# Kernel optimization log

Measured on AMD Instinct MI355X. Metric: run time of the kernel, lower is better.

## Reference

```python
import jax, jax.numpy as jnp
import numpy as np

L, N, D_IN = 4, 2048, 1024
H, DH = 8, 64
INNER = H * DH          # 512
D_OUT = D_IN            # out_dim defaults to input_dim
SCALE = DH ** -0.5


def setup_inputs() -> dict:
    key = jax.random.key(0)
    ks = jax.random.split(key, 7)
    x = jax.random.normal(ks[0], (L, N, D_IN), jnp.float32)
    # torch Linear weights are [out_features, in_features]; xavier-ish scale
    Wq = jax.random.normal(ks[1], (INNER, D_IN), jnp.float32) * 0.03
    Wk = jax.random.normal(ks[2], (INNER, D_IN), jnp.float32) * 0.03
    Wv = jax.random.normal(ks[3], (INNER, D_IN), jnp.float32) * 0.03
    Wo = jax.random.normal(ks[4], (D_OUT, INNER), jnp.float32) * 0.03
    bo = jnp.zeros((D_OUT,), jnp.float32)
    # boolean key-padding mask [L, n]; ensure at least one valid key per row
    mask = jax.random.uniform(ks[5], (L, N)) < 0.9
    mask = mask.at[:, 0].set(True)
    return {"x": x, "Wq": Wq, "Wk": Wk, "Wv": Wv, "Wo": Wo, "bo": bo, "mask": mask}


def reference(x, Wq, Wk, Wv, Wo, bo, mask):
    # projections (Linear: y = x @ W^T), split heads: L n (h d) -> l h n d
    def split_heads(t):
        return t.reshape(L, N, H, DH).transpose(0, 2, 1, 3)

    q = split_heads(jnp.einsum('lnd,ed->lne', x, Wq))
    k = split_heads(jnp.einsum('lnd,ed->lne', x, Wk))  # context defaults to x
    v = split_heads(jnp.einsum('lnd,ed->lne', x, Wv))

    sim = jnp.einsum('lhnd,lhmd->lhnm', q, k) * SCALE   # [L,H,N,N]
    neg = -jnp.finfo(sim.dtype).max
    sim = jnp.where(mask[:, None, None, :], sim, neg)   # mask over key dim
    attn = jax.nn.softmax(sim, axis=-1)

    out = jnp.einsum('lhnm,lhmd->lhnd', attn, v)        # [L,H,N,DH]
    out = out.transpose(0, 2, 1, 3).reshape(L, N, INNER)
    return out @ Wo.T + bo                               # [L,N,D_OUT]
```

## Files before the change

kernel.cpp:

```cpp
#include <hip/hip_runtime.h>
#include <hip/hip_bf16.h>

#define L_DIM 4
#define N_DIM 2048
#define DIN   1024
#define H_DIM 8
#define DH    64
#define INNER 512

typedef __attribute__((ext_vector_type(8))) short short8;
typedef __attribute__((ext_vector_type(4))) float f32x4;

__device__ __forceinline__ unsigned short f2bf(float f) {
  unsigned u = __builtin_bit_cast(unsigned, f);
  u += 0x7fffu + ((u >> 16) & 1u);
  return (unsigned short)(u >> 16);
}

__device__ __forceinline__ unsigned cvtpk(float a, float b) {
  unsigned r;
  asm("v_cvt_pk_bf16_f32 %0, %1, %2" : "=v"(r) : "v"(a), "v"(b));
  return r;
}

__device__ __forceinline__ float fexp2(float x) {
  float r;
  asm("v_exp_f32 %0, %1" : "=v"(r) : "v"(x));
  return r;
}

typedef __attribute__((address_space(3))) unsigned int lds_uint;
typedef const __attribute__((address_space(1))) unsigned int glob_uint;
__device__ __forceinline__ void gl_lds16(const unsigned short* g,
                                         unsigned short* l) {
  __builtin_amdgcn_global_load_lds((glob_uint*)g, (lds_uint*)l, 16, 0, 0);
}

__global__ void cast_all(const float* __restrict__ x,
                         const float* __restrict__ wq,
                         const float* __restrict__ wk,
                         const float* __restrict__ wv,
                         const float* __restrict__ wo,
                         unsigned short* __restrict__ xb,
                         unsigned short* __restrict__ w3,
                         unsigned short* __restrict__ wob,
                         const unsigned char* __restrict__ mraw,
                         float* __restrict__ bias) {
  __shared__ int votes[2];
  int bid = blockIdx.x, t = threadIdx.x;
  if (bid == 10240) {
    if (t < 2) votes[t] = 0;
    __syncthreads();
    const unsigned int* m32 = (const unsigned int*)mraw;
    int anyf = 0, any8 = 0;
    for (int i = t; i < 2048; i += 256) {
      unsigned w = m32[i];
      if (w == 0x3f800000u) anyf = 1;
      if (w & 0xffffff00u) any8 = 1;
    }
    if (anyf) atomicOr(&votes[0], 1);
    if (any8) atomicOr(&votes[1], 1);
    __syncthreads();
    int fmt = votes[0] ? 2 : (votes[1] ? 1 : 0);
    for (int i = t; i < L_DIM * N_DIM; i += 256) {
      int mv;
      if (fmt == 2)      mv = ((const float*)mraw)[i] != 0.0f;
      else if (fmt == 1) mv = mraw[i] != 0;
      else               mv = ((const int*)mraw)[i] != 0;
      bias[i] = mv ? 0.0f : -1e30f;
    }
    return;
  }
  int i = (bid * 256 + t) * 4;
  const float* src; unsigned short* dst; int off;
  if (i < 8388608)      { src = x;  dst = xb;           off = i; }
  else if (i < 8912896) { src = wq; dst = w3;           off = i - 8388608; }
  else if (i < 9437184) { src = wk; dst = w3 + 524288;  off = i - 8912896; }
  else if (i < 9961472) { src = wv; dst = w3 + 1048576; off = i - 9437184; }
  else                  { src = wo; dst = wob;          off = i - 9961472; }
  float4 f = *(const float4*)(src + off);
  ushort4 o4;
  o4.x = f2bf(f.x); o4.y = f2bf(f.y); o4.z = f2bf(f.z); o4.w = f2bf(f.w);
  *(ushort4*)(dst + off) = o4;
}

__launch_bounds__(256, 3)
__global__ void gemm_qkv(const unsigned short* __restrict__ xb,
                         const unsigned short* __restrict__ w3,
                         unsigned short* __restrict__ qp,
                         unsigned short* __restrict__ kp,
                         unsigned short* __restrict__ vtp) {
  __shared__ __align__(16) unsigned short Sh[16384];
  const int tid = threadIdx.x, lane = tid & 63, wid = tid >> 6;
  const int l16 = lane & 15, quad = lane >> 4;
  const int wm = wid >> 1, wn = wid & 1;
  const int m0 = blockIdx.x * 128, n0 = blockIdx.y * 128;

  int aoff[2], boff[2], lofs[2];
#pragma unroll
  for (int it = 0; it < 2; ++it) {
    int c = it * 256 + wid * 64 + lane;
    int row = c >> 2, kseg = c & 3;
    aoff[it] = (m0 + row) * DIN + kseg * 8;
    boff[it] = (n0 + row) * DIN + kseg * 8;
    lofs[it] = (it * 256 + wid * 64) * 8;
  }

#pragma unroll
  for (int it = 0; it < 2; ++it) {
    gl_lds16(&xb[aoff[it]], &Sh[lofs[it]]);
    gl_lds16(&w3[boff[it]], &Sh[8192 + lofs[it]]);
  }

  f32x4 acc[4][4] = {};
  for (int t = 0; t < 32; ++t) {
    const int buf = t & 1;
    __syncthreads();
    if (t < 31) {
      int kt2 = (t + 1) * 32, b2 = buf ^ 1;
#pragma unroll
      for (int it = 0; it < 2; ++it) {
        gl_lds16(&xb[aoff[it] + kt2], &Sh[b2 * 4096 + lofs[it]]);
        gl_lds16(&w3[boff[it] + kt2], &Sh[8192 + b2 * 4096 + lofs[it]]);
      }
    }
    const unsigned short* As = &Sh[buf * 4096];
    const unsigned short* Bs = &Sh[8192 + buf * 4096];
    short8 af[4], bf[4];
#pragma unroll
    for (int mt = 0; mt < 4; ++mt)
      af[mt] = *(const short8*)&As[(wm * 64 + mt * 16 + l16) * 32 + quad * 8];
#pragma unroll
    for (int nt = 0; nt < 4; ++nt)
      bf[nt] = *(const short8*)&Bs[(wn * 64 + nt * 16 + l16) * 32 + quad * 8];
#pragma unroll
    for (int mt = 0; mt < 4; ++mt)
#pragma unroll
      for (int nt = 0; nt < 4; ++nt)
        acc[mt][nt] = __builtin_amdgcn_mfma_f32_16x16x32_bf16(
            af[mt], bf[nt], acc[mt][nt], 0, 0, 0);
  }
  if (blockIdx.y >= 8) {
    const int l = m0 >> 11, mloc = m0 & 2047;
#pragma unroll
    for (int chunk = 0; chunk < 2; ++chunk) {
      __syncthreads();
      if (wn == chunk) {
#pragma unroll
        for (int mt = 0; mt < 4; ++mt)
#pragma unroll
          for (int nt = 0; nt < 4; ++nt) {
            int col = nt * 16 + l16;
            int rowb = wm * 64 + mt * 16 + quad * 4;
            ushort4 pv;
            pv.x = f2bf(acc[mt][nt][0]);
            pv.y = f2bf(acc[mt][nt][1]);
            pv.z = f2bf(acc[mt][nt][2]);
            pv.w = f2bf(acc[mt][nt][3]);
            *(ushort4*)&Sh[col * 136 + rowb] = pv;
          }
      }
      __syncthreads();
      int hh = ((n0 + chunk * 64) & 511) >> 6;
#pragma unroll
      for (int it = 0; it < 4; ++it) {
        int c = it * 256 + tid;
        int cl = c >> 4, seg = c & 15;
        short8 vv = *(const short8*)&Sh[cl * 136 + seg * 8];
        *(short8*)&vtp[((size_t)((l * H_DIM + hh) * DH + cl)) * N_DIM + mloc +
                       seg * 8] = vv;
      }
    }
  } else {
    const int l = m0 >> 11, nloc = m0 & 2047;
    const int hbase = (n0 & 511) >> 6;
    unsigned short* dstp = (n0 >> 9) ? kp : qp;
#pragma unroll
    for (int chunk = 0; chunk < 2; ++chunk) {
      __syncthreads();
      if (wn == chunk) {
#pragma unroll
        for (int mt = 0; mt < 4; ++mt)
#pragma unroll
          for (int nt = 0; nt < 4; ++nt) {
            int col = nt * 16 + l16;
            int rowb = wm * 64 + mt * 16 + quad * 4;
#pragma unroll
            for (int r = 0; r < 4; ++r)
              Sh[(rowb + r) * 72 + col] = f2bf(acc[mt][nt][r]);
          }
      }
      __syncthreads();
      int hh = hbase + chunk;
      unsigned short* db =
          dstp + ((size_t)(l * H_DIM + hh) * N_DIM + nloc) * DH;
#pragma unroll
      for (int it = 0; it < 4; ++it) {
        int c = it * 256 + tid;
        int row = c >> 3, seg = c & 7;
        short8 vv = *(const short8*)&Sh[row * 72 + seg * 8];
        *(short8*)&db[row * DH + seg * 8] = vv;
      }
    }
  }
}

#define PW_S 64
__launch_bounds__(128, 2)
__global__ void attn_kernel(const unsigned short* __restrict__ qg,
                            const unsigned short* __restrict__ kg,
                            const unsigned short* __restrict__ vtg,
                            const float* __restrict__ bias,
                            unsigned short* __restrict__ aout) {
  __shared__ __align__(16) unsigned short Ks[2][64 * 64];
  __shared__ __align__(16) unsigned short Vs[2][64 * 64];
  __shared__ __align__(16) unsigned short Pw[64 * PW_S];
  const int tid = threadIdx.x, lane = tid & 63, wid = tid >> 6;
  const int l16 = lane & 15, quad = lane >> 4;
  const int bid = blockIdx.x;
  const int xcd = bid & 7, j = bid >> 3;
  const int lh = xcd * 4 + (j >> 5);
  const int q0 = (j & 31) << 6;
  const int l = lh >> 3, h = lh & 7;
  const unsigned short* Qb = qg + (size_t)lh * N_DIM * DH;
  const unsigned short* Kb = kg + (size_t)lh * N_DIM * DH;
  const unsigned short* Vt = vtg + (size_t)lh * DH * N_DIM;
  const float* bl = bias + l * N_DIM;

  short8 qf[2][2];
#pragma unroll
  for (int mt = 0; mt < 2; ++mt)
#pragma unroll
    for (int ks = 0; ks < 2; ++ks)
      qf[mt][ks] = *(const short8*)&Qb[(q0 + wid * 32 + mt * 16 + l16) * DH +
                                       ks * 32 + quad * 8];

  f32x4 o[2][4] = {};
  float lsum[2] = {0.f, 0.f};

  int kof[4], ldsb[4];
  size_t vof[4];
#pragma unroll
  for (int it = 0; it < 4; ++it) {
    int cb = it * 128 + wid * 64, c = cb + lane;
    int rr = c >> 3, sl = c & 7, gs = (sl + rr) & 7;
    kof[it] = rr * DH + gs * 8;
    vof[it] = (size_t)rr * N_DIM + gs * 8;
    ldsb[it] = cb * 8;
  }

#pragma unroll
  for (int it = 0; it < 4; ++it) {
    gl_lds16(&Kb[kof[it]], &Ks[0][ldsb[it]]);
    gl_lds16(&Vt[vof[it]], &Vs[0][ldsb[it]]);
  }

  for (int t = 0; t < 32; ++t) {
    const int kv = t << 6, buf = t & 1;
    __syncthreads();
    if (t < 31) {
      int kv2 = kv + 64, b2 = buf ^ 1;
#pragma unroll
      for (int it = 0; it < 4; ++it) {
        gl_lds16(&Kb[(kv2 << 6) + kof[it]], &Ks[b2][ldsb[it]]);
        gl_lds16(&Vt[vof[it] + kv2], &Vs[b2][ldsb[it]]);
      }
    }
    const unsigned short* Kst = Ks[buf];
    const unsigned short* Vst = Vs[buf];

    f32x4 sc[2][4] = {};
#pragma unroll
    for (int nt = 0; nt < 4; ++nt)
#pragma unroll
      for (int ks = 0; ks < 2; ++ks) {
        int s = (ks * 4 + quad - l16) & 7;
        short8 kf = *(const short8*)&Kst[(nt * 16 + l16) * 64 + s * 8];
#pragma unroll
        for (int mt = 0; mt < 2; ++mt)
          sc[mt][nt] = __builtin_amdgcn_mfma_f32_16x16x32_bf16(
              kf, qf[mt][ks], sc[mt][nt], 0, 0, 0);
      }
#pragma unroll
    for (int mt = 0; mt < 2; ++mt) {
      unsigned short* pr = &Pw[(wid * 32 + mt * 16 + l16) * PW_S];
#pragma unroll
      for (int nt = 0; nt < 4; ++nt) {
        float4 b4 = *(const float4*)&bl[kv + nt * 16 + quad * 4];
        float p0 = fexp2(fmaf(sc[mt][nt][0], 0.18033688011f, b4.x));
        float p1 = fexp2(fmaf(sc[mt][nt][1], 0.18033688011f, b4.y));
        float p2 = fexp2(fmaf(sc[mt][nt][2], 0.18033688011f, b4.z));
        float p3 = fexp2(fmaf(sc[mt][nt][3], 0.18033688011f, b4.w));
        lsum[mt] += (p0 + p1) + (p2 + p3);
        uint2 pk = make_uint2(cvtpk(p0, p1), cvtpk(p2, p3));
        int gk = nt * 2 + (quad >> 1);
        int s = (gk + l16) & 7;
        *(uint2*)&pr[s * 8 + (quad & 1) * 4] = pk;
      }
    }
#pragma unroll
    for (int g = 0; g < 2; ++g) {
      short8 pa[2];
#pragma unroll
      for (int mt = 0; mt < 2; ++mt) {
        int sp = (g * 4 + quad + l16) & 7;
        pa[mt] = *(const short8*)&Pw[(wid * 32 + mt * 16 + l16) * PW_S +
                                     sp * 8];
      }
#pragma unroll
      for (int nt = 0; nt < 4; ++nt) {
        int dd = nt * 16 + l16;
        int sv2 = (g * 4 + quad - l16) & 7;
        short8 vb = *(const short8*)&Vst[dd * 64 + sv2 * 8];
#pragma unroll
        for (int mt = 0; mt < 2; ++mt)
          o[mt][nt] = __builtin_amdgcn_mfma_f32_16x16x32_bf16(
              pa[mt], vb, o[mt][nt], 0, 0, 0);
      }
    }
  }
#pragma unroll
  for (int mt = 0; mt < 2; ++mt) {
    lsum[mt] += __shfl_xor(lsum[mt], 16);
    lsum[mt] += __shfl_xor(lsum[mt], 32);
  }
#pragma unroll
  for (int mt = 0; mt < 2; ++mt)
#pragma unroll
    for (int r = 0; r < 4; ++r) {
      float inv = 1.f / __shfl(lsum[mt], quad * 4 + r);
      int row = q0 + wid * 32 + mt * 16 + quad * 4 + r;
#pragma unroll
      for (int nt = 0; nt < 4; ++nt)
        aout[(size_t)(l * N_DIM + row) * INNER + h * DH + nt * 16 + l16] =
            f2bf(o[mt][nt][r] * inv);
    }
}

__launch_bounds__(256, 4)
__global__ void gemm_out(const unsigned short* __restrict__ a,
                         const unsigned short* __restrict__ wo,
                         const float* __restrict__ bo,
                         float* __restrict__ out) {
  __shared__ __align__(16) unsigned short Sh[12288];
  const int tid = threadIdx.x, lane = tid & 63, wid = tid >> 6;
  const int l16 = lane & 15, quad = lane >> 4;
  const int wm = wid >> 1, wn = wid & 1;
  const int m0 = blockIdx.x * 128, n0 = blockIdx.y * 64;

  int aoff[2], lofsA[2];
#pragma unroll
  for (int it = 0; it < 2; ++it) {
    int c = it * 256 + wid * 64 + lane;
    int row = c >> 2, kseg = c & 3;
    aoff[it] = (m0 + row) * INNER + kseg * 8;
    lofsA[it] = (it * 256 + wid * 64) * 8;
  }
  int boff, lofsB;
  {
    int c = wid * 64 + lane;
    int row = c >> 2, kseg = c & 3;
    boff = (n0 + row) * INNER + kseg * 8;
    lofsB = (wid * 64) * 8;
  }

#pragma unroll
  for (int it = 0; it < 2; ++it)
    gl_lds16(&a[aoff[it]], &Sh[lofsA[it]]);
  gl_lds16(&wo[boff], &Sh[8192 + lofsB]);

  f32x4 acc[4][2] = {};
  for (int t = 0; t < 16; ++t) {
    const int buf = t & 1;
    __syncthreads();
    if (t < 15) {
      int kt2 = (t + 1) * 32, b2 = buf ^ 1;
#pragma unroll
      for (int it = 0; it < 2; ++it)
        gl_lds16(&a[aoff[it] + kt2], &Sh[b2 * 4096 + lofsA[it]]);
      gl_lds16(&wo[boff + kt2], &Sh[8192 + b2 * 2048 + lofsB]);
    }
    const unsigned short* As = &Sh[buf * 4096];
    const unsigned short* Bs = &Sh[8192 + buf * 2048];
    short8 af[4], bf[2];
#pragma unroll
    for (int mt = 0; mt < 4; ++mt)
      af[mt] = *(const short8*)&As[(wm * 64 + mt * 16 + l16) * 32 + quad * 8];
#pragma unroll
    for (int nt = 0; nt < 2; ++nt)
      bf[nt] = *(const short8*)&Bs[(wn * 32 + nt * 16 + l16) * 32 + quad * 8];
#pragma unroll
    for (int mt = 0; mt < 4; ++mt)
#pragma unroll
      for (int nt = 0; nt < 2; ++nt)
        acc[mt][nt] = __builtin_amdgcn_mfma_f32_16x16x32_bf16(
            af[mt], bf[nt], acc[mt][nt], 0, 0, 0);
  }
#pragma unroll
  for (int mt = 0; mt < 4; ++mt)
#pragma unroll
    for (int nt = 0; nt < 2; ++nt)
#pragma unroll
      for (int r = 0; r < 4; ++r) {
        int grow = m0 + wm * 64 + mt * 16 + quad * 4 + r;
        int gcol = n0 + wn * 32 + nt * 16 + l16;
        out[(size_t)grow * DIN + gcol] = acc[mt][nt][r] + bo[gcol];
      }
}

extern "C" void kernel_launch(void* const* d_in, const int* in_sizes, int n_in,
                              void* d_out, int out_size, void* d_ws,
                              size_t ws_size, hipStream_t stream) {
  const float* x  = (const float*)d_in[0];
  const float* Wq = (const float*)d_in[1];
  const float* Wk = (const float*)d_in[2];
  const float* Wv = (const float*)d_in[3];
  const float* Wo = (const float*)d_in[4];
  const float* bo = (const float*)d_in[5];
  const unsigned char* mask = (const unsigned char*)d_in[6];
  float* out = (float*)d_out;

  char* ws = (char*)d_ws;
  unsigned short* xb  = (unsigned short*)(ws + 0);
  unsigned short* w3  = (unsigned short*)(ws + 16777216);
  unsigned short* wob = (unsigned short*)(ws + 19922944);
  unsigned short* q   = (unsigned short*)(ws + 20971520);
  unsigned short* k   = (unsigned short*)(ws + 29360128);
  unsigned short* vt  = (unsigned short*)(ws + 37748736);
  unsigned short* att = (unsigned short*)(ws + 46137344);
  float* bias         = (float*)(ws + 54525952);

  cast_all<<<10241, 256, 0, stream>>>(x, Wq, Wk, Wv, Wo, xb, w3, wob, mask,
                                      bias);
  gemm_qkv<<<dim3(64, 12), 256, 0, stream>>>(xb, w3, q, k, vt);
  attn_kernel<<<1024, 128, 0, stream>>>(q, k, vt, bias, att);
  gemm_out<<<dim3(64, 16), 256, 0, stream>>>(att, wob, bo, out);
}
```

Baseline: 218.0 us.

## Halve attention query and key/value tiles to double block count and occupancy

Shrinks the attention block from 64 queries to 32 (16 per wave) and the key/value tile from 64 to 32, doubling the grid to 2048 blocks. It raises occupancy to 4 blocks per CU and cuts LDS and register use per block. In exchange each K/V tile is reused by half as many queries, so global and LDS traffic for K/V doubles and the loop runs twice as many barrier iterations.

```diff
diff --git a/kernel.cpp b/kernel.cpp
--- a/kernel.cpp
+++ b/kernel.cpp
@@ -205,63 +205,64 @@
   }
 }
 
-#define PW_S 64
-__launch_bounds__(128, 2)
+#define KVB 32
+#define PW_S 32
+__launch_bounds__(128, 4)
 __global__ void attn_kernel(const unsigned short* __restrict__ qg,
                             const unsigned short* __restrict__ kg,
                             const unsigned short* __restrict__ vtg,
                             const float* __restrict__ bias,
                             unsigned short* __restrict__ aout) {
-  __shared__ __align__(16) unsigned short Ks[2][64 * 64];
-  __shared__ __align__(16) unsigned short Vs[2][64 * 64];
-  __shared__ __align__(16) unsigned short Pw[64 * PW_S];
+  __shared__ __align__(16) unsigned short Ks[2][KVB * 64];
+  __shared__ __align__(16) unsigned short Vs[2][64 * KVB];
+  __shared__ __align__(16) unsigned short Pw[32 * PW_S];
   const int tid = threadIdx.x, lane = tid & 63, wid = tid >> 6;
   const int l16 = lane & 15, quad = lane >> 4;
   const int bid = blockIdx.x;
   const int xcd = bid & 7, j = bid >> 3;
-  const int lh = xcd * 4 + (j >> 5);
-  const int q0 = (j & 31) << 6;
+  const int lh = xcd * 4 + (j >> 6);
+  const int q0 = (j & 63) << 5;
   const int l = lh >> 3, h = lh & 7;
   const unsigned short* Qb = qg + (size_t)lh * N_DIM * DH;
   const unsigned short* Kb = kg + (size_t)lh * N_DIM * DH;
   const unsigned short* Vt = vtg + (size_t)lh * DH * N_DIM;
   const float* bl = bias + l * N_DIM;
 
-  short8 qf[2][2];
-#pragma unroll
-  for (int mt = 0; mt < 2; ++mt)
-#pragma unroll
-    for (int ks = 0; ks < 2; ++ks)
-      qf[mt][ks] = *(const short8*)&Qb[(q0 + wid * 32 + mt * 16 + l16) * DH +
-                                       ks * 32 + quad * 8];
-
-  f32x4 o[2][4] = {};
-  float lsum[2] = {0.f, 0.f};
-
-  int kof[4], ldsb[4];
-  size_t vof[4];
-#pragma unroll
-  for (int it = 0; it < 4; ++it) {
-    int cb = it * 128 + wid * 64, c = cb + lane;
-    int rr = c >> 3, sl = c & 7, gs = (sl + rr) & 7;
-    kof[it] = rr * DH + gs * 8;
-    vof[it] = (size_t)rr * N_DIM + gs * 8;
-    ldsb[it] = cb * 8;
-  }
-
-#pragma unroll
-  for (int it = 0; it < 4; ++it) {
+  short8 qf[2];
+#pragma unroll
+  for (int ks = 0; ks < 2; ++ks)
+    qf[ks] = *(const short8*)&Qb[(q0 + wid * 16 + l16) * DH + ks * 32 +
+                                 quad * 8];
+
+  f32x4 o[4] = {};
+  float lsum = 0.f;
+
+  int kof[2], vof0[2], ldsb[2];
+  size_t vof[2];
+#pragma unroll
+  for (int it = 0; it < 2; ++it) {
+    int c = it * 128 + wid * 64 + lane;
+    int key = c >> 3, sl = c & 7, gs = (sl + key) & 7;
+    kof[it] = key * DH + gs * 8;
+    int d = c >> 2, sv = c & 3, gv = (sv + d) & 3;
+    vof[it] = (size_t)d * N_DIM + gv * 8;
+    ldsb[it] = c * 8;
+  }
+  (void)vof0;
+
+#pragma unroll
+  for (int it = 0; it < 2; ++it) {
     gl_lds16(&Kb[kof[it]], &Ks[0][ldsb[it]]);
     gl_lds16(&Vt[vof[it]], &Vs[0][ldsb[it]]);
   }
 
-  for (int t = 0; t < 32; ++t) {
-    const int kv = t << 6, buf = t & 1;
+  for (int t = 0; t < 64; ++t) {
+    const int kv = t << 5, buf = t & 1;
     __syncthreads();
-    if (t < 31) {
-      int kv2 = kv + 64, b2 = buf ^ 1;
-#pragma unroll
-      for (int it = 0; it < 4; ++it) {
+    if (t < 63) {
+      int kv2 = kv + KVB, b2 = buf ^ 1;
+#pragma unroll
+      for (int it = 0; it < 2; ++it) {
         gl_lds16(&Kb[(kv2 << 6) + kof[it]], &Ks[b2][ldsb[it]]);
         gl_lds16(&Vt[vof[it] + kv2], &Vs[b2][ldsb[it]]);
       }
@@ -269,72 +270,54 @@
     const unsigned short* Kst = Ks[buf];
     const unsigned short* Vst = Vs[buf];
 
-    f32x4 sc[2][4] = {};
-#pragma unroll
-    for (int nt = 0; nt < 4; ++nt)
+    f32x4 sc[2] = {};
+#pragma unroll
+    for (int nt = 0; nt < 2; ++nt)
 #pragma unroll
       for (int ks = 0; ks < 2; ++ks) {
         int s = (ks * 4 + quad - l16) & 7;
         short8 kf = *(const short8*)&Kst[(nt * 16 + l16) * 64 + s * 8];
-#pragma unroll
-        for (int mt = 0; mt < 2; ++mt)
-          sc[mt][nt] = __builtin_amdgcn_mfma_f32_16x16x32_bf16(
-              kf, qf[mt][ks], sc[mt][nt], 0, 0, 0);
-      }
-#pragma unroll
-    for (int mt = 0; mt < 2; ++mt) {
-      unsigned short* pr = &Pw[(wid * 32 + mt * 16 + l16) * PW_S];
-#pragma unroll
-      for (int nt = 0; nt < 4; ++nt) {
-        float4 b4 = *(const float4*)&bl[kv + nt * 16 + quad * 4];
-        float p0 = fexp2(fmaf(sc[mt][nt][0], 0.18033688011f, b4.x));
-        float p1 = fexp2(fmaf(sc[mt][nt][1], 0.18033688011f, b4.y));
-        float p2 = fexp2(fmaf(sc[mt][nt][2], 0.18033688011f, b4.z));
-        float p3 = fexp2(fmaf(sc[mt][nt][3], 0.18033688011f, b4.w));
-        lsum[mt] += (p0 + p1) + (p2 + p3);
-        uint2 pk = make_uint2(cvtpk(p0, p1), cvtpk(p2, p3));
-        int gk = nt * 2 + (quad >> 1);
-        int s = (gk + l16) & 7;
-        *(uint2*)&pr[s * 8 + (quad & 1) * 4] = pk;
-      }
-    }
-#pragma unroll
-    for (int g = 0; g < 2; ++g) {
-      short8 pa[2];
-#pragma unroll
-      for (int mt = 0; mt < 2; ++mt) {
-        int sp = (g * 4 + quad + l16) & 7;
-        pa[mt] = *(const short8*)&Pw[(wid * 32 + mt * 16 + l16) * PW_S +
-                                     sp * 8];
-      }
+        sc[nt] = __builtin_amdgcn_mfma_f32_16x16x32_bf16(kf, qf[ks], sc[nt],
+                                                         0, 0, 0);
+      }
+    unsigned short* pr = &Pw[(wid * 16 + l16) * PW_S];
+#pragma unroll
+    for (int nt = 0; nt < 2; ++nt) {
+      float4 b4 = *(const float4*)&bl[kv + nt * 16 + quad * 4];
+      float p0 = fexp2(fmaf(sc[nt][0], 0.18033688011f, b4.x));
+      float p1 = fexp2(fmaf(sc[nt][1], 0.18033688011f, b4.y));
+      float p2 = fexp2(fmaf(sc[nt][2], 0.18033688011f, b4.z));
+      float p3 = fexp2(fmaf(sc[nt][3], 0.18033688011f, b4.w));
+      lsum += (p0 + p1) + (p2 + p3);
+      uint2 pkv = make_uint2(cvtpk(p0, p1), cvtpk(p2, p3));
+      int gk = nt * 2 + (quad >> 1);
+      int s = (gk + l16) & 3;
+      *(uint2*)&pr[s * 8 + (quad & 1) * 4] = pkv;
+    }
+    {
+      int sp = (quad + l16) & 3;
+      short8 pa = *(const short8*)&Pw[(wid * 16 + l16) * PW_S + sp * 8];
 #pragma unroll
       for (int nt = 0; nt < 4; ++nt) {
         int dd = nt * 16 + l16;
-        int sv2 = (g * 4 + quad - l16) & 7;
-        short8 vb = *(const short8*)&Vst[dd * 64 + sv2 * 8];
-#pragma unroll
-        for (int mt = 0; mt < 2; ++mt)
-          o[mt][nt] = __builtin_amdgcn_mfma_f32_16x16x32_bf16(
-              pa[mt], vb, o[mt][nt], 0, 0, 0);
-      }
-    }
-  }
-#pragma unroll
-  for (int mt = 0; mt < 2; ++mt) {
-    lsum[mt] += __shfl_xor(lsum[mt], 16);
-    lsum[mt] += __shfl_xor(lsum[mt], 32);
-  }
-#pragma unroll
-  for (int mt = 0; mt < 2; ++mt)
-#pragma unroll
-    for (int r = 0; r < 4; ++r) {
-      float inv = 1.f / __shfl(lsum[mt], quad * 4 + r);
-      int row = q0 + wid * 32 + mt * 16 + quad * 4 + r;
-#pragma unroll
-      for (int nt = 0; nt < 4; ++nt)
-        aout[(size_t)(l * N_DIM + row) * INNER + h * DH + nt * 16 + l16] =
-            f2bf(o[mt][nt][r] * inv);
-    }
+        int sv2 = (quad - l16) & 3;
+        short8 vb = *(const short8*)&Vst[dd * KVB + sv2 * 8];
+        o[nt] = __builtin_amdgcn_mfma_f32_16x16x32_bf16(pa, vb, o[nt],
+                                                        0, 0, 0);
+      }
+    }
+  }
+  lsum += __shfl_xor(lsum, 16);
+  lsum += __shfl_xor(lsum, 32);
+#pragma unroll
+  for (int r = 0; r < 4; ++r) {
+    float inv = 1.f / __shfl(lsum, quad * 4 + r);
+    int row = q0 + wid * 16 + quad * 4 + r;
+#pragma unroll
+    for (int nt = 0; nt < 4; ++nt)
+      aout[(size_t)(l * N_DIM + row) * INNER + h * DH + nt * 16 + l16] =
+          f2bf(o[nt][r] * inv);
+  }
 }
 
 __launch_bounds__(256, 4)
@@ -433,6 +416,6 @@
   cast_all<<<10241, 256, 0, stream>>>(x, Wq, Wk, Wv, Wo, xb, w3, wob, mask,
                                       bias);
   gemm_qkv<<<dim3(64, 12), 256, 0, stream>>>(xb, w3, q, k, vt);
-  attn_kernel<<<1024, 128, 0, stream>>>(q, k, vt, bias, att);
+  attn_kernel<<<2048, 128, 0, stream>>>(q, k, vt, bias, att);
   gemm_out<<<dim3(64, 16), 256, 0, stream>>>(att, wob, bo, out);
 }
```

Result: slower. 225.2 us (+3.3%).
